# Optimization experiments

Hardware: AMD Instinct MI355X
Metric: run time of the kernel (lower is better)

## Reference

```python
import jax, jax.numpy as jnp
import numpy as np

N, E, D = 50000, 640000, 128


def setup_inputs() -> dict:
    key = jax.random.key(0)
    ks = jax.random.split(key, 10)
    scale = (2.0 / (D + D)) ** 0.5  # xavier-ish scale for square weights

    def w(k):
        return jax.random.normal(k, (D, D), jnp.float32) * scale

    return {
        "x": jax.random.normal(ks[0], (N, D), jnp.float32),
        "view2": jax.random.normal(ks[1], (N, D), jnp.float32),
        "W_neigh1": w(ks[2]),
        "W_self1": w(ks[3]),
        "b_self1": jnp.zeros((D,), jnp.float32),
        "W_neigh2": w(ks[4]),
        "W_self2": w(ks[5]),
        "b_self2": jnp.zeros((D,), jnp.float32),
        "W_attn": w(ks[6]),
        "b_attn": jnp.zeros((D,), jnp.float32),
        "att": jax.random.normal(ks[7], (1, D), jnp.float32) * 0.1,
        "src": jax.random.randint(ks[8], (E,), 0, N),
        "dst": jax.random.randint(ks[9], (E,), 0, N),
    }


def _sage_mean(h, src, dst, W_neigh, W_self, b_self, n):
    """DGL SAGEConv, aggregator_type='mean', in_feats==out_feats (lin after mp)."""
    msgs = h[src]  # gather: [E, D]
    s = jax.ops.segment_sum(msgs, dst, num_segments=n)  # scatter-add: [N, D]
    deg = jax.ops.segment_sum(jnp.ones((src.shape[0],), h.dtype), dst, num_segments=n)
    h_neigh = jnp.where(deg[:, None] > 0, s / jnp.maximum(deg, 1.0)[:, None], 0.0)
    # rst = fc_self(h_self) + fc_neigh(h_neigh)
    return h @ W_self.T + b_self + h_neigh @ W_neigh.T


def reference(x, view2, W_neigh1, W_self1, b_self1, W_neigh2, W_self2, b_self2,
              W_attn, b_attn, att, src, dst):
    n = x.shape[0]
    # SAGENet: outs = [h, l1(h)/1, l2(l1(h))/2]; res = sum(outs)
    h1 = _sage_mean(x, src, dst, W_neigh1, W_self1, b_self1, n)
    h2 = _sage_mean(h1, src, dst, W_neigh2, W_self2, b_self2, n)
    res = x + h1 + h2 * 0.5
    # Attn semantic fusion over embedding views [res, view2]
    embeds = (res, view2)
    scores = jnp.stack(
        [att[0] @ jnp.tanh(e @ W_attn.T + b_attn).mean(axis=0) for e in embeds]
    )  # [2]
    beta = jax.nn.softmax(scores)
    return beta[0] * res + beta[1] * view2
```

## Files before the change

kernel.cpp:

```cpp
#include <hip/hip_runtime.h>

#define DD 128

using bf16 = __bf16;
typedef __bf16 bf16x8 __attribute__((ext_vector_type(8)));
typedef float f32x4 __attribute__((ext_vector_type(4)));
typedef float f32x2 __attribute__((ext_vector_type(2)));

__device__ inline bf16x8 cvt8(const float* p) {
  f32x4 v0 = *(const f32x4*)p;
  f32x4 v1 = *(const f32x4*)(p + 4);
  bf16x8 r;
  r[0] = (bf16)v0[0]; r[1] = (bf16)v0[1]; r[2] = (bf16)v0[2]; r[3] = (bf16)v0[3];
  r[4] = (bf16)v1[0]; r[5] = (bf16)v1[1]; r[6] = (bf16)v1[2]; r[7] = (bf16)v1[3];
  return r;
}

__device__ inline uint2 pk8fp8(const float* f) {
  int u0 = __builtin_amdgcn_cvt_pk_fp8_f32(f[0], f[1], 0, 0);
  u0 = __builtin_amdgcn_cvt_pk_fp8_f32(f[2], f[3], u0, 1);
  int u1 = __builtin_amdgcn_cvt_pk_fp8_f32(f[4], f[5], 0, 0);
  u1 = __builtin_amdgcn_cvt_pk_fp8_f32(f[6], f[7], u1, 1);
  uint2 r; r.x = (unsigned)u0; r.y = (unsigned)u1; return r;
}

__device__ inline void acc4fp8(unsigned w, float* a) {
  f32x2 p;
  p = __builtin_amdgcn_cvt_pk_f32_fp8(w, 0); a[0] += p.x; a[1] += p.y;
  p = __builtin_amdgcn_cvt_pk_f32_fp8(w, 1); a[2] += p.x; a[3] += p.y;
}

__device__ inline float ftanh(float x) {
  float e2 = __expf(2.0f * x);
  return 1.0f - 2.0f * __builtin_amdgcn_rcpf(e2 + 1.0f);
}

__device__ inline int swz(int o) { return o ^ (((o >> 8) & 7) << 4); }

__global__ void k_prep(int* __restrict__ cnt, int N,
                       const float* __restrict__ w0, const float* __restrict__ w1,
                       const float* __restrict__ w2, const float* __restrict__ w3,
                       const float* __restrict__ w4, bf16* __restrict__ wb, int totalW,
                       const float* __restrict__ x, bf16* __restrict__ xb,
                       unsigned char* __restrict__ xb8, int total8,
                       int nbZ, int nbW) {
  int b = blockIdx.x;
  if (b < nbZ) {
    int i = b * 256 + threadIdx.x;
    if (i < N) cnt[i] = 0;
  } else if (b < nbZ + nbW) {
    int i = (b - nbZ) * 256 + threadIdx.x;
    if (i < totalW) {
      int m = i >> 14;
      int r = i & 16383;
      const float* s = m == 0 ? w0 : m == 1 ? w1 : m == 2 ? w2 : m == 3 ? w3 : w4;
      wb[i] = (bf16)s[r];
    }
  } else {
    int i = (b - nbZ - nbW) * 256 + threadIdx.x;
    if (i < total8) {
      float f[8];
      f32x4 v0 = *(const f32x4*)(x + (size_t)i * 8);
      f32x4 v1 = *(const f32x4*)(x + (size_t)i * 8 + 4);
#pragma unroll
      for (int j = 0; j < 4; ++j) { f[j] = v0[j]; f[4 + j] = v1[j]; }
      bf16x8 r;
#pragma unroll
      for (int j = 0; j < 8; ++j) r[j] = (bf16)f[j];
      *(bf16x8*)(xb + (size_t)i * 8) = r;
      *(uint2*)(xb8 + (size_t)i * 8) = pk8fp8(f);
    }
  }
}

__global__ void k_cvt8(const bf16* __restrict__ h, unsigned char* __restrict__ h8,
                       int total8) {
  int i = blockIdx.x * 256 + threadIdx.x;
  if (i >= total8) return;
  bf16x8 v = *(const bf16x8*)(h + (size_t)i * 8);
  float f[8];
#pragma unroll
  for (int j = 0; j < 8; ++j) f[j] = (float)v[j];
  *(uint2*)(h8 + (size_t)i * 8) = pk8fp8(f);
}

__global__ void k_hist(const int* __restrict__ dst, int* __restrict__ cnt,
                       int E, int N) {
  int p = blockIdx.x & 7;
  int slice = blockIdx.x >> 3;
  int nslice = gridDim.x >> 3;
  int lo = p * (N >> 3);
  int hi = (p == 7) ? N : lo + (N >> 3);
  for (int e = slice * 256 + threadIdx.x; e < E; e += nslice * 256) {
    int d = dst[e];
    if (d >= lo && d < hi) atomicAdd(&cnt[d], 1);
  }
}

__global__ void k_scatter(const int* __restrict__ src, const int* __restrict__ dst,
                          int* __restrict__ cursor, int* __restrict__ ssrc,
                          int E, int N) {
  int p = blockIdx.x & 7;
  int slice = blockIdx.x >> 3;
  int nslice = gridDim.x >> 3;
  int lo = p * (N >> 3);
  int hi = (p == 7) ? N : lo + (N >> 3);
  for (int e = slice * 256 + threadIdx.x; e < E; e += nslice * 256) {
    int d = dst[e];
    if (d >= lo && d < hi) {
      int pos = atomicAdd(&cursor[d], 1);
      ssrc[pos] = src[e];
    }
  }
}

__global__ __launch_bounds__(256) void k_scan1(const int* __restrict__ cnt,
                                               int* __restrict__ bsum, int N) {
  __shared__ int sm[256];
  int t = threadIdx.x;
  int i = blockIdx.x * 256 + t;
  sm[t] = (i < N) ? cnt[i] : 0;
  __syncthreads();
#pragma unroll
  for (int d = 128; d > 0; d >>= 1) {
    if (t < d) sm[t] += sm[t + d];
    __syncthreads();
  }
  if (t == 0) bsum[blockIdx.x] = sm[0];
}

__global__ __launch_bounds__(256) void k_scan2(int* __restrict__ bsum, int nb) {
  __shared__ int sm[256];
  int t = threadIdx.x;
  int v = (t < nb) ? bsum[t] : 0;
  sm[t] = v;
  __syncthreads();
#pragma unroll
  for (int d = 1; d < 256; d <<= 1) {
    int u = (t >= d) ? sm[t - d] : 0;
    __syncthreads();
    sm[t] += u;
    __syncthreads();
  }
  if (t < nb) bsum[t] = sm[t] - v;
}

__global__ __launch_bounds__(256) void k_scan3(const int* __restrict__ cnt,
                                               const int* __restrict__ bsum,
                                               int* __restrict__ offs,
                                               int* __restrict__ cursor, int N) {
  __shared__ int sm[256];
  int t = threadIdx.x;
  int i = blockIdx.x * 256 + t;
  int v = (i < N) ? cnt[i] : 0;
  sm[t] = v;
  __syncthreads();
#pragma unroll
  for (int d = 1; d < 256; d <<= 1) {
    int u = (t >= d) ? sm[t - d] : 0;
    __syncthreads();
    sm[t] += u;
    __syncthreads();
  }
  int incl = sm[t];
  int base = bsum[blockIdx.x];
  if (i < N) {
    int ex = base + incl - v;
    offs[i] = ex;
    cursor[i] = ex;
    if (i == N - 1) offs[N] = base + incl;
  }
}

template <int MODE>
__global__ __launch_bounds__(1024, 1) void k_layer(const bf16* __restrict__ Hb,
                                                   const unsigned char* __restrict__ Hb8,
                                                   const int* __restrict__ offs,
                                                   const int* __restrict__ ssrc,
                                                   const bf16* __restrict__ Wsb,
                                                   const bf16* __restrict__ Wnb,
                                                   const float* __restrict__ bias,
                                                   const float* __restrict__ Xres,
                                                   bf16* __restrict__ H1out,
                                                   bf16* __restrict__ Resb, int N) {
  __shared__ char smem[65536];
  int t = threadIdx.x;
#pragma unroll
  for (int m = 0; m < 2; ++m) {
    const bf16* wsrc = m ? Wnb : Wsb;
#pragma unroll
    for (int it = 0; it < 2; ++it) {
      int o = (it * 1024 + t) * 16;
      *(bf16x8*)(smem + m * 32768 + swz(o)) = *(const bf16x8*)(wsrc + o / 2);
    }
  }
  __syncthreads();

  int wv = t >> 6;
  int lane = t & 63;
  int tile = wv * gridDim.x + blockIdx.x;
  int n0 = tile << 4;
  if (n0 >= N) return;
  int lr = lane & 15;
  int g = lane >> 4;

  int node = n0 + lr;

  const bf16* a1p = Hb + (size_t)node * DD + g * 32;
  bf16x8 a1[4];
#pragma unroll
  for (int kk = 0; kk < 4; ++kk) a1[kk] = *(const bf16x8*)(a1p + kk * 8);

  int beg = offs[node], end = offs[node + 1];
  float acc[4][8];
#pragma unroll
  for (int kk = 0; kk < 4; ++kk)
#pragma unroll
    for (int j = 0; j < 8; ++j) acc[kk][j] = 0.f;
  for (int i = beg; i < end; ++i) {
    int s = ssrc[i];
    const unsigned char* hp = Hb8 + (size_t)s * DD + g * 32;
    uint4 u0 = *(const uint4*)(hp);
    uint4 u1 = *(const uint4*)(hp + 16);
    acc4fp8(u0.x, &acc[0][0]); acc4fp8(u0.y, &acc[0][4]);
    acc4fp8(u0.z, &acc[1][0]); acc4fp8(u0.w, &acc[1][4]);
    acc4fp8(u1.x, &acc[2][0]); acc4fp8(u1.y, &acc[2][4]);
    acc4fp8(u1.z, &acc[3][0]); acc4fp8(u1.w, &acc[3][4]);
  }
  float inv = (end > beg) ? 1.0f / (float)(end - beg) : 0.f;
  bf16x8 a2[4];
#pragma unroll
  for (int kk = 0; kk < 4; ++kk)
#pragma unroll
    for (int j = 0; j < 8; ++j) a2[kk][j] = (bf16)(acc[kk][j] * inv);

  int rb = n0 + (g << 2);
#pragma unroll
  for (int j = 0; j < 8; ++j) {
    int row = j * 16 + lr;
    int rbase = row * 256 + g * 64;
    f32x4 cs = {0.f, 0.f, 0.f, 0.f};
    f32x4 cn = {0.f, 0.f, 0.f, 0.f};
#pragma unroll
    for (int kk = 0; kk < 4; ++kk) {
      int ro = swz(rbase + kk * 16);
      bf16x8 bs = *(const bf16x8*)(smem + ro);
      bf16x8 bn = *(const bf16x8*)(smem + 32768 + ro);
      cs = __builtin_amdgcn_mfma_f32_16x16x32_bf16(a1[kk], bs, cs, 0, 0, 0);
      cn = __builtin_amdgcn_mfma_f32_16x16x32_bf16(a2[kk], bn, cn, 0, 0, 0);
    }
    int col = j * 16 + lr;
    float bb = bias[col];
#pragma unroll
    for (int r = 0; r < 4; ++r) {
      size_t idx = (size_t)(rb + r) * DD + col;
      float v = cs[r] + cn[r] + bb;
      if (MODE == 0) H1out[idx] = (bf16)v;
      else           Resb[idx] = (bf16)(Xres[idx] + (float)Hb[idx] + 0.5f * v);
    }
  }
}

__global__ __launch_bounds__(512, 4) void k_attn2(const bf16* __restrict__ resb,
                                                  const float* __restrict__ v2f,
                                                  const bf16* __restrict__ Wab,
                                                  const float* __restrict__ bias,
                                                  const float* __restrict__ att,
                                                  float* __restrict__ partial,
                                                  int nbA, int N) {
  __shared__ char smem[32768];
  __shared__ float smr[8];
  int t = threadIdx.x;
#pragma unroll
  for (int it = 0; it < 4; ++it) {
    int o = (it * 512 + t) * 16;
    *(bf16x8*)(smem + swz(o)) = *(const bf16x8*)(Wab + o / 2);
  }
  __syncthreads();

  int wv = t >> 6;
  int lane = t & 63;
  int gwid = blockIdx.x * 8 + wv;
  int view = gwid & 1;
  int tile = gwid >> 1;
  int n0 = tile << 4;
  float part = 0.f;
  if (n0 < N) {
    int lr = lane & 15;
    int lk = (lane >> 4) << 3;
    bf16x8 a[4];
    if (view) {
      const float* ap = v2f + (size_t)(n0 + lr) * DD + lk;
#pragma unroll
      for (int kk = 0; kk < 4; ++kk) a[kk] = cvt8(ap + kk * 32);
    } else {
      const bf16* ap = resb + (size_t)(n0 + lr) * DD + lk;
#pragma unroll
      for (int kk = 0; kk < 4; ++kk) a[kk] = *(const bf16x8*)(ap + kk * 32);
    }
#pragma unroll
    for (int j = 0; j < 8; ++j) {
      int row = j * 16 + lr;
      int rbase = row * 256 + lk * 2;
      f32x4 c = {0.f, 0.f, 0.f, 0.f};
#pragma unroll
      for (int kk = 0; kk < 4; ++kk) {
        bf16x8 bw = *(const bf16x8*)(smem + swz(rbase + kk * 64));
        c = __builtin_amdgcn_mfma_f32_16x16x32_bf16(a[kk], bw, c, 0, 0, 0);
      }
      int col = j * 16 + lr;
      float aw = att[col], bb = bias[col];
#pragma unroll
      for (int r = 0; r < 4; ++r) part += aw * ftanh(c[r] + bb);
    }
  }
#pragma unroll
  for (int d = 1; d < 64; d <<= 1) part += __shfl_xor(part, d);
  if (lane == 0) smr[wv] = part;
  __syncthreads();
  if (t == 0) {
    partial[blockIdx.x]       = smr[0] + smr[2] + smr[4] + smr[6];
    partial[nbA + blockIdx.x] = smr[1] + smr[3] + smr[5] + smr[7];
  }
}

__global__ __launch_bounds__(256) void k_score(const float* __restrict__ partial,
                                               float* __restrict__ scores, int nbA) {
  __shared__ float sm[256];
  int t = threadIdx.x;
#pragma unroll
  for (int v = 0; v < 2; ++v) {
    float s = 0.f;
    for (int i = t; i < nbA; i += 256) s += partial[v * nbA + i];
    sm[t] = s;
    __syncthreads();
#pragma unroll
    for (int d = 128; d > 0; d >>= 1) {
      if (t < d) sm[t] += sm[t + d];
      __syncthreads();
    }
    if (t == 0) scores[v] = sm[0];
    __syncthreads();
  }
}

__global__ void k_fin(float* __restrict__ out, const bf16* __restrict__ resb,
                      const float* __restrict__ v2,
                      const float* __restrict__ scores, float invN, int total8) {
  int i = blockIdx.x * 256 + threadIdx.x;
  if (i >= total8) return;
  float s0 = scores[0] * invN, s1 = scores[1] * invN;
  float m = fmaxf(s0, s1);
  float e0 = expf(s0 - m), e1 = expf(s1 - m);
  float inv = 1.0f / (e0 + e1);
  float b0 = e0 * inv, b1 = e1 * inv;
  bf16x8 r = ((const bf16x8*)resb)[i];
  f32x4 w0 = ((const f32x4*)v2)[2 * i];
  f32x4 w1 = ((const f32x4*)v2)[2 * i + 1];
  f32x4 o0, o1;
#pragma unroll
  for (int j = 0; j < 4; ++j) {
    o0[j] = b0 * (float)r[j] + b1 * w0[j];
    o1[j] = b0 * (float)r[4 + j] + b1 * w1[j];
  }
  ((f32x4*)out)[2 * i] = o0;
  ((f32x4*)out)[2 * i + 1] = o1;
}

extern "C" void kernel_launch(void* const* d_in, const int* in_sizes, int n_in,
                              void* d_out, int out_size, void* d_ws, size_t ws_size,
                              hipStream_t stream) {
  const float* x   = (const float*)d_in[0];
  const float* v2  = (const float*)d_in[1];
  const float* Wn1 = (const float*)d_in[2];
  const float* Ws1 = (const float*)d_in[3];
  const float* b1  = (const float*)d_in[4];
  const float* Wn2 = (const float*)d_in[5];
  const float* Ws2 = (const float*)d_in[6];
  const float* b2  = (const float*)d_in[7];
  const float* Wa  = (const float*)d_in[8];
  const float* ba  = (const float*)d_in[9];
  const float* att = (const float*)d_in[10];
  const int*  src  = (const int*)d_in[11];
  const int*  dst  = (const int*)d_in[12];
  const int D = in_sizes[4];
  const int N = in_sizes[0] / D;
  const int E = in_sizes[11];
  float* out = (float*)d_out;

  char* ws = (char*)d_ws;
  size_t o = 0;
  auto alloc = [&](size_t bytes) -> void* {
    void* p = ws + o;
    o += (bytes + 255) & ~(size_t)255;
    return p;
  };
  int*  cnt    = (int*)alloc((size_t)N * 4);
  int*  offs   = (int*)alloc((size_t)(N + 1) * 4);
  int*  cursor = (int*)alloc((size_t)N * 4);
  int*  ssrc   = (int*)alloc((size_t)E * 4);
  bf16* xb     = (bf16*)alloc((size_t)N * D * 2);
  bf16* h1b    = (bf16*)alloc((size_t)N * D * 2);
  bf16* resb   = (bf16*)alloc((size_t)N * D * 2);
  unsigned char* xb8  = (unsigned char*)alloc((size_t)N * D);
  unsigned char* h1b8 = (unsigned char*)alloc((size_t)N * D);
  bf16* wb     = (bf16*)alloc((size_t)5 * D * D * 2);
  float* sc    = (float*)alloc(2 * 4);
  int nb = (N + 255) / 256;
  int*  bsum   = (int*)alloc((size_t)nb * 4);

  int tilesPerView = (N + 15) / 16;
  int attnWaves = 2 * tilesPerView;
  int nbA = (attnWaves + 7) / 8;
  float* apart = (float*)alloc((size_t)2 * nbA * 4);

  int nbZ = (N + 255) / 256;
  int nbW = (5 * D * D + 255) / 256;
  int nbX = (N * D / 8 + 255) / 256;
  k_prep<<<nbZ + nbW + nbX, 256, 0, stream>>>(cnt, N, Ws1, Wn1, Ws2, Wn2, Wa, wb,
                                              5 * D * D, x, xb, xb8, N * D / 8,
                                              nbZ, nbW);

  k_hist<<<2048, 256, 0, stream>>>(dst, cnt, E, N);
  k_scan1<<<nb, 256, 0, stream>>>(cnt, bsum, N);
  k_scan2<<<1, 256, 0, stream>>>(bsum, nb);
  k_scan3<<<nb, 256, 0, stream>>>(cnt, bsum, offs, cursor, N);
  k_scatter<<<2048, 256, 0, stream>>>(src, dst, cursor, ssrc, E, N);

  int layerBlocks = 256;

  k_layer<0><<<layerBlocks, 1024, 0, stream>>>(xb, xb8, offs, ssrc, wb, wb + D * D,
                                               b1, nullptr, h1b, nullptr, N);
  k_cvt8<<<(N * D / 8 + 255) / 256, 256, 0, stream>>>(h1b, h1b8, N * D / 8);
  k_layer<1><<<layerBlocks, 1024, 0, stream>>>(h1b, h1b8, offs, ssrc, wb + 2 * D * D,
                                               wb + 3 * D * D, b2, x, nullptr, resb, N);
  k_attn2<<<nbA, 512, 0, stream>>>(resb, v2, wb + 4 * D * D, ba, att, apart, nbA, N);
  k_score<<<1, 256, 0, stream>>>(apart, sc, nbA);
  k_fin<<<((N * D / 8) + 255) / 256, 256, 0, stream>>>(out, resb, v2, sc,
                                                       1.0f / (float)N, N * D / 8);
}
```

Before: 166.9 us.

## Fuse fp8 conversion into layer-1 epilogue via permuted h1 column layout

Layer 1 now stores h1 in a permuted column order so that each lane writes 8 contiguous bf16 values and their fp8 copy directly from the MFMA epilogue. This removes the separate k_cvt8 kernel and its extra read of h1. To keep results consistent, the layer-2 weights are column-permuted during prep and the layer-2 residual read indexes h1 through the permutation. The residual read in layer 2 becomes a strided gather, and the permutation has to match exactly across all three sites.

After: 162.3 us. 2.7% less time.

```diff
diff --git a/kernel.cpp b/kernel.cpp
--- a/kernel.cpp
+++ b/kernel.cpp
@@ -54,7 +54,12 @@
       int m = i >> 14;
       int r = i & 16383;
       const float* s = m == 0 ? w0 : m == 1 ? w1 : m == 2 ? w2 : m == 3 ? w3 : w4;
-      wb[i] = (bf16)s[r];
+      int srcIdx = r;
+      if (m == 2 || m == 3) {
+        int row = r >> 7, p = r & 127;
+        srcIdx = row * 128 + ((p & 7) * 16 + (p >> 3));
+      }
+      wb[i] = (bf16)s[srcIdx];
     }
   } else {
     int i = (b - nbZ - nbW) * 256 + threadIdx.x;
@@ -71,17 +76,6 @@
       *(uint2*)(xb8 + (size_t)i * 8) = pk8fp8(f);
     }
   }
-}
-
-__global__ void k_cvt8(const bf16* __restrict__ h, unsigned char* __restrict__ h8,
-                       int total8) {
-  int i = blockIdx.x * 256 + threadIdx.x;
-  if (i >= total8) return;
-  bf16x8 v = *(const bf16x8*)(h + (size_t)i * 8);
-  float f[8];
-#pragma unroll
-  for (int j = 0; j < 8; ++j) f[j] = (float)v[j];
-  *(uint2*)(h8 + (size_t)i * 8) = pk8fp8(f);
 }
 
 __global__ void k_hist(const int* __restrict__ dst, int* __restrict__ cnt,
@@ -182,6 +176,7 @@
                                                    const float* __restrict__ bias,
                                                    const float* __restrict__ Xres,
                                                    bf16* __restrict__ H1out,
+                                                   unsigned char* __restrict__ H1out8,
                                                    bf16* __restrict__ Resb, int N) {
   __shared__ char smem[65536];
   int t = threadIdx.x;
@@ -235,6 +230,7 @@
     for (int j = 0; j < 8; ++j) a2[kk][j] = (bf16)(acc[kk][j] * inv);
 
   int rb = n0 + (g << 2);
+  f32x4 vreg[8];
 #pragma unroll
   for (int j = 0; j < 8; ++j) {
     int row = j * 16 + lr;
@@ -252,11 +248,29 @@
     int col = j * 16 + lr;
     float bb = bias[col];
 #pragma unroll
+    for (int r = 0; r < 4; ++r) vreg[j][r] = cs[r] + cn[r] + bb;
+  }
+
+  if (MODE == 0) {
+#pragma unroll
     for (int r = 0; r < 4; ++r) {
-      size_t idx = (size_t)(rb + r) * DD + col;
-      float v = cs[r] + cn[r] + bb;
-      if (MODE == 0) H1out[idx] = (bf16)v;
-      else           Resb[idx] = (bf16)(Xres[idx] + (float)Hb[idx] + 0.5f * v);
+      float f[8]; bf16x8 hb;
+#pragma unroll
+      for (int j = 0; j < 8; ++j) { f[j] = vreg[j][r]; hb[j] = (bf16)f[j]; }
+      size_t base = (size_t)(rb + r) * DD + lr * 8;
+      *(bf16x8*)(H1out + base) = hb;
+      *(uint2*)(H1out8 + base) = pk8fp8(f);
+    }
+  } else {
+#pragma unroll
+    for (int j = 0; j < 8; ++j) {
+      int col = j * 16 + lr;
+#pragma unroll
+      for (int r = 0; r < 4; ++r) {
+        size_t row = (size_t)(rb + r);
+        float h1v = (float)Hb[row * DD + lr * 8 + j];
+        Resb[row * DD + col] = (bf16)(Xres[row * DD + col] + h1v + 0.5f * vreg[j][r]);
+      }
     }
   }
 }
@@ -430,10 +444,10 @@
   int layerBlocks = 256;
 
   k_layer<0><<<layerBlocks, 1024, 0, stream>>>(xb, xb8, offs, ssrc, wb, wb + D * D,
-                                               b1, nullptr, h1b, nullptr, N);
-  k_cvt8<<<(N * D / 8 + 255) / 256, 256, 0, stream>>>(h1b, h1b8, N * D / 8);
+                                               b1, nullptr, h1b, h1b8, nullptr, N);
   k_layer<1><<<layerBlocks, 1024, 0, stream>>>(h1b, h1b8, offs, ssrc, wb + 2 * D * D,
-                                               wb + 3 * D * D, b2, x, nullptr, resb, N);
+                                               wb + 3 * D * D, b2, x, nullptr, nullptr,
+                                               resb, N);
   k_attn2<<<nbA, 512, 0, stream>>>(resb, v2, wb + 4 * D * D, ba, att, apart, nbA, N);
   k_score<<<1, 256, 0, stream>>>(apart, sc, nbA);
   k_fin<<<((N * D / 8) + 255) / 256, 256, 0, stream>>>(out, resb, v2, sc,
```
